# Kernel tuning notes

Measured on AMD Instinct MI355X. Metric: run time of the kernel, lower is better.

## Reference

```python
import jax, jax.numpy as jnp
import numpy as np

N = 10000      # nodes per graph
E = 160000     # random edges per graph (plus N self-loops)
IN_DIM = 4096
HID = 64       # num_hidden
H = 8          # heads
C = 5          # num_classes
SLOPE = 0.2    # LeakyReLU negative slope


def gat_conv(x, src, dst, W, al, ar, b, res_W=None):
    """DGL-style GATConv. x:(N,F) -> (N,H,D). Messages flow src->dst,
    edge softmax over in-edges of each dst node."""
    n = x.shape[0]
    h, d = al.shape
    feat = (x @ W).reshape(n, h, d)                      # (N,H,D)
    el = jnp.sum(feat * al, axis=-1)                     # (N,H)
    er = jnp.sum(feat * ar, axis=-1)                     # (N,H)
    e = jax.nn.leaky_relu(el[src] + er[dst], SLOPE)      # (E,H)
    emax = jax.ops.segment_max(e, dst, num_segments=n)   # (N,H) stable softmax
    ex = jnp.exp(e - emax[dst])
    denom = jax.ops.segment_sum(ex, dst, num_segments=n)
    alpha = ex / denom[dst]                              # (E,H)
    out = jax.ops.segment_sum(feat[src] * alpha[..., None], dst, num_segments=n)
    if res_W is not None:
        out = out + (x @ res_W).reshape(n, h, d)         # residual projection
    return out + b.reshape(h, d)


def encoder(x, src, dst, W0, al0, ar0, b0, W1, al1, ar1, b1):
    h0 = jax.nn.elu(gat_conv(x, src, dst, W0, al0, ar0, b0))   # (N,H,D)
    h0 = h0.reshape(h0.shape[0], -1)                           # flatten(1)
    return jax.nn.elu(gat_conv(h0, src, dst, W1, al1, ar1, b1))


def setup_inputs() -> dict:
    key = jax.random.key(0)
    ks = list(jax.random.split(key, 40))
    ki = iter(ks)

    def edges(k):
        k1, k2 = jax.random.split(k)
        loop = jnp.arange(N, dtype=jnp.int32)
        s = jnp.concatenate([jax.random.randint(k1, (E,), 0, N, dtype=jnp.int32), loop])
        d = jnp.concatenate([jax.random.randint(k2, (E,), 0, N, dtype=jnp.int32), loop])
        return s, d

    inp = {}
    for name in ("s0", "s1", "t"):
        s, d = edges(next(ki))
        inp[f"src_{name}"], inp[f"dst_{name}"] = s, d
    inp["features_s0"] = jax.random.normal(next(ki), (N, IN_DIM), jnp.float32)
    inp["features_s1"] = jax.random.normal(next(ki), (N, IN_DIM), jnp.float32)
    inp["features_t"]  = jax.random.normal(next(ki), (N, IN_DIM), jnp.float32)

    def lin(k, fan_in, fan_out):
        return jax.random.normal(k, (fan_in, fan_out), jnp.float32) / np.sqrt(fan_in)

    inp["W0"] = lin(next(ki), IN_DIM, H * HID)
    inp["al0"] = 0.1 * jax.random.normal(next(ki), (H, HID), jnp.float32)
    inp["ar0"] = 0.1 * jax.random.normal(next(ki), (H, HID), jnp.float32)
    inp["b0"] = jnp.zeros((H * HID,), jnp.float32)
    inp["W1"] = lin(next(ki), H * HID, H * HID)
    inp["al1"] = 0.1 * jax.random.normal(next(ki), (H, HID), jnp.float32)
    inp["ar1"] = 0.1 * jax.random.normal(next(ki), (H, HID), jnp.float32)
    inp["b1"] = jnp.zeros((H * HID,), jnp.float32)
    for k_idx in (0, 1):
        inp[f"Wc{k_idx}"] = lin(next(ki), H * HID, H * C)
        inp[f"alc{k_idx}"] = 0.1 * jax.random.normal(next(ki), (H, C), jnp.float32)
        inp[f"arc{k_idx}"] = 0.1 * jax.random.normal(next(ki), (H, C), jnp.float32)
        inp[f"bc{k_idx}"] = jnp.zeros((H * C,), jnp.float32)
        inp[f"rW{k_idx}"] = lin(next(ki), H * HID, H * C)
    inp["num_source"] = 2
    return inp


def reference(features_s0, features_s1, features_t,
              W0, al0, ar0, b0, W1, al1, ar1, b1,
              Wc0, alc0, arc0, bc0, rW0,
              Wc1, alc1, arc1, bc1, rW1,
              src_s0, dst_s0, src_s1, dst_s1, src_t, dst_t,
              num_source):
    enc_p = (W0, al0, ar0, b0, W1, al1, ar1, b1)
    cls_p = [(Wc0, alc0, arc0, bc0, rW0), (Wc1, alc1, arc1, bc1, rW1)]
    feats = [features_s0, features_s1]
    graphs = [(src_s0, dst_s0), (src_s1, dst_s1)]

    # shared-weight encoder on each source graph
    h_s = [encoder(feats[i], graphs[i][0], graphs[i][1], *enc_p)
           for i in range(num_source)]                    # each (N,H,HID)
    # per-source classifiers on their own graphs, mean over heads
    pred_s = []
    for i in range(num_source):
        Wc, alc, arc, bc, rW = cls_p[i]
        s, d = graphs[i]
        logits = gat_conv(h_s[i].reshape(N, -1), s, d, Wc, alc, arc, bc, res_W=rW)
        pred_s.append(logits.mean(axis=1))               # (N,C)
    emb_s = [h.reshape(N, -1) for h in h_s]

    # target: every source classifier applied to the target graph
    h_t = encoder(features_t, src_t, dst_t, *enc_p)
    pred_t = []
    for i in range(num_source):
        Wc, alc, arc, bc, rW = cls_p[i]
        logits = gat_conv(h_t.reshape(N, -1), src_t, dst_t, Wc, alc, arc, bc, res_W=rW)
        pred_t.append(logits.mean(axis=1))
    emb_t = h_t.reshape(N, -1)

    return (pred_s[0], pred_s[1], pred_t[0], pred_t[1], emb_s[0], emb_s[1], emb_t)
```

## Files before the change

### kernel.cpp

```cpp
#include <hip/hip_runtime.h>
#include <stdint.h>

typedef _Float16 f16;
typedef _Float16 f16x2 __attribute__((ext_vector_type(2)));
typedef _Float16 f16x8 __attribute__((ext_vector_type(8)));
typedef float f32x4 __attribute__((ext_vector_type(4)));

#define AS1 __attribute__((address_space(1)))
#define AS3 __attribute__((address_space(3)))

#define NN 10000
#define NP 10112
#define KK0 4096
#define FF 512

__global__ void k_count_b(const int* __restrict__ d0, const int* __restrict__ d1,
                          const int* __restrict__ d2, int E0, int E1, int E2,
                          int nb0, int nb1, int* __restrict__ deg){
  int b = blockIdx.x;
  const int* d; int Eg, base, lb;
  if (b < nb0){ d=d0; Eg=E0; base=0; lb=b; }
  else if (b < nb0+nb1){ d=d1; Eg=E1; base=NN; lb=b-nb0; }
  else { d=d2; Eg=E2; base=2*NN; lb=b-nb0-nb1; }
  int i = lb*256 + threadIdx.x;
  if (i < Eg) atomicAdd(&deg[base + d[i]], 1);
}

__global__ __launch_bounds__(1024) void k_scan_b(const int* __restrict__ deg_all,
    int* __restrict__ rowptr_all, int* __restrict__ cursor_all){
  int g = blockIdx.x;
  const int* deg = deg_all + g*NN;
  int* rowptr = rowptr_all + g*(NN+1);
  int* cursor = cursor_all + g*NN;
  __shared__ int ps[1024];
  int t = threadIdx.x;
  const int CH = 16;
  int i0 = t*CH;
  int sum = 0;
  for (int k=0;k<CH;k++){ int i=i0+k; if (i<NN) sum += deg[i]; }
  ps[t]=sum; __syncthreads();
  for (int off=1; off<1024; off<<=1){
    int v = (t>=off)? ps[t-off] : 0;
    __syncthreads();
    ps[t] += v;
    __syncthreads();
  }
  int run = ps[t]-sum;
  for (int k=0;k<CH;k++){
    int i=i0+k;
    if (i<=NN) rowptr[i]=run;
    if (i<NN){ cursor[i]=run; run += deg[i]; }
  }
}

__global__ void k_fill_b(const int* __restrict__ s0, const int* __restrict__ d0,
                         const int* __restrict__ s1, const int* __restrict__ d1,
                         const int* __restrict__ s2, const int* __restrict__ d2,
                         int E0, int E1, int E2, int nb0, int nb1,
                         int* __restrict__ cursor_all,
                         int* __restrict__ c0, int* __restrict__ c1, int* __restrict__ c2){
  int b = blockIdx.x;
  const int *s, *d; int Eg, lb; int* cur; int* col;
  if (b < nb0){ s=s0; d=d0; Eg=E0; lb=b; cur=cursor_all; col=c0; }
  else if (b < nb0+nb1){ s=s1; d=d1; Eg=E1; lb=b-nb0; cur=cursor_all+NN; col=c1; }
  else { s=s2; d=d2; Eg=E2; lb=b-nb0-nb1; cur=cursor_all+2*NN; col=c2; }
  int i = lb*256 + threadIdx.x;
  if (i >= Eg) return;
  int slot = atomicAdd(&cur[d[i]], 1);
  col[slot] = s[i];
}

__global__ void k_transpose_t(const float* __restrict__ W, f16* __restrict__ WT,
                              int K, int Nc){
  __shared__ float tile[32][33];
  int n0 = blockIdx.x*32, k0 = blockIdx.y*32;
  int tx = threadIdx.x, ty = threadIdx.y;
  #pragma unroll
  for (int i=0;i<32;i+=8)
    tile[ty+i][tx] = W[(long)(k0+ty+i)*Nc + n0+tx];
  __syncthreads();
  #pragma unroll
  for (int i=0;i<32;i+=8)
    WT[(long)(n0+ty+i)*K + k0+tx] = (f16)tile[tx][ty+i];
}

__global__ void k_pack_wc(const float* __restrict__ Wc, const float* __restrict__ rW,
                          f16* __restrict__ WT){
  int idx = blockIdx.x*256 + threadIdx.x;
  if (idx >= 128*512) return;
  int n = idx >> 9; int k = idx & 511;
  float v = 0.f;
  if (n < 40) v = Wc[k*40 + n];
  else if (n < 80) v = rW[k*40 + (n-40)];
  WT[idx] = (f16)v;
}

template<bool CVT>
__global__ __launch_bounds__(512,1) void k_gemmw(
    const void* __restrict__ A0v, const void* __restrict__ A1v, const void* __restrict__ A2v,
    f16* __restrict__ C0, f16* __restrict__ C1, f16* __restrict__ C2,
    const f16* __restrict__ B,
    const float* __restrict__ alp, const float* __restrict__ arp,
    float* __restrict__ elp, float* __restrict__ erp)
{
  constexpr int K = CVT ? KK0 : FF;
  constexpr int nt = K >> 6;
  __shared__ f16 lds[2][40960];

  const int nwg = gridDim.x;
  const int qd = nwg>>3, rd = nwg&7;
  const int xcd = blockIdx.x & 7, bx = blockIdx.x >> 3;
  const int wid = (xcd < rd ? xcd*(qd+1) : rd*(qd+1) + (xcd-rd)*qd) + bx;
  const int task = wid / 79;
  const int tr = wid - task*79;

  f16* C = task==0?C0:(task==1?C1:C2);

  const int t = threadIdx.x;
  const int wave = t >> 6, lane = t & 63;
  const int slot = (lane&7) ^ (lane>>3);
  const int arow0 = t >> 3;
  const int ak8 = t & 7;

  #define GLDSB_H(kt, buf, half) { \
    int ko = (kt)*64; \
    _Pragma("unroll") \
    for (int i=(half)*4; i<(half)*4+4; i++){ \
      int br = i*64 + wave*8 + (lane>>3); \
      __builtin_amdgcn_global_load_lds((const AS1 void*)(B + (long)br*K + ko + slot*8), \
          (AS3 void*)(&lds[buf][8192 + i*4096 + wave*512]), 16, 0, 0); \
    } }
  #define GLDSB(kt, buf) { GLDSB_H(kt, buf, 0); GLDSB_H(kt, buf, 1); }

  int abyte[2][8], bbyte[2][4];
  #pragma unroll
  for (int ks=0;ks<2;ks++){
    #pragma unroll
    for (int m=0;m<8;m++){
      int row = m*16 + (lane&15);
      abyte[ks][m] = row*128 + (((ks*4 + (lane>>4))*16) ^ ((row&7)<<4));
    }
    #pragma unroll
    for (int n=0;n<4;n++){
      int brow = wave*64 + n*16 + (lane&15);
      bbyte[ks][n] = 16384 + brow*128 + (((ks*4 + (lane>>4))*16) ^ ((brow&7)<<4));
    }
  }

  f32x4 zero4 = {0.f,0.f,0.f,0.f};
  f32x4 acc[8][4];
  #pragma unroll
  for (int m=0;m<8;m++)
    #pragma unroll
    for (int n=0;n<4;n++) acc[m][n] = zero4;

  #define MFMA_KS(buf, ks) { \
    const char* Ls = (const char*)&lds[buf][0]; \
    f16x8 bf[4]; \
    _Pragma("unroll") \
    for (int n=0;n<4;n++) bf[n] = *(const f16x8*)(Ls + bbyte[ks][n]); \
    _Pragma("unroll") \
    for (int m=0;m<8;m++){ \
      f16x8 af = *(const f16x8*)(Ls + abyte[ks][m]); \
      _Pragma("unroll") \
      for (int n=0;n<4;n++) \
        acc[m][n] = __builtin_amdgcn_mfma_f32_16x16x32_f16(af, bf[n], acc[m][n], 0, 0, 0); \
    } }

  int cur = 0;
  if constexpr (CVT){
    const float* Af = task==0?(const float*)A0v:(task==1?(const float*)A1v:(const float*)A2v);
    const float* gA[2];
    bool okA[2];
    #pragma unroll
    for (int s=0;s<2;s++){
      int grow = tr*128 + arow0 + s*64;
      okA[s] = grow < NN;
      gA[s] = Af + (long)(okA[s] ? grow : 0)*KK0 + ak8*8;
    }
    f32x4 arE[2][2];

    #define LOADA(kt) { \
      _Pragma("unroll") \
      for (int s=0;s<2;s++){ \
        arE[s][0] = *(const f32x4*)(gA[s] + (kt)*64); \
        arE[s][1] = *(const f32x4*)(gA[s] + (kt)*64 + 4); \
      } }
    #define WRITEA(buf) { \
      _Pragma("unroll") \
      for (int s=0;s<2;s++){ \
        int row = arow0 + s*64; \
        f16x8 v; \
        _Pragma("unroll") \
        for (int j=0;j<4;j++){ \
          v[j]   = okA[s] ? (f16)arE[s][0][j] : (f16)0.f; \
          v[4+j] = okA[s] ? (f16)arE[s][1][j] : (f16)0.f; \
        } \
        *(f16x8*)(&lds[buf][row*64 + ((ak8 ^ (arow0&7))*8)]) = v; \
      } }

    LOADA(0);
    __builtin_amdgcn_sched_barrier(0);
    GLDSB(0, 0);
    __builtin_amdgcn_sched_barrier(0);
    WRITEA(0);
    __builtin_amdgcn_sched_barrier(0);
    LOADA(1);
    __builtin_amdgcn_sched_barrier(0);
    asm volatile("s_waitcnt vmcnt(4) lgkmcnt(0)" ::: "memory");
    __builtin_amdgcn_s_barrier();
    __builtin_amdgcn_sched_barrier(0);

    for (int kt=0; kt<nt; kt++){
      if (kt+1 < nt){
        GLDSB_H(kt+1, cur^1, 0);
        __builtin_amdgcn_sched_barrier(0);
        WRITEA(cur^1);
        __builtin_amdgcn_sched_barrier(0);
      }
      __builtin_amdgcn_s_setprio(1);
      MFMA_KS(cur, 0);
      __builtin_amdgcn_s_setprio(0);
      __builtin_amdgcn_sched_barrier(0);
      if (kt+1 < nt){
        GLDSB_H(kt+1, cur^1, 1);
        __builtin_amdgcn_sched_barrier(0);
      }
      if (kt+2 < nt){
        LOADA(kt+2);
        __builtin_amdgcn_sched_barrier(0);
      }
      __builtin_amdgcn_s_setprio(1);
      MFMA_KS(cur, 1);
      __builtin_amdgcn_s_setprio(0);
      __builtin_amdgcn_sched_barrier(0);
      if (kt+1 < nt){
        if (kt+2 < nt)
          asm volatile("s_waitcnt vmcnt(4) lgkmcnt(0)" ::: "memory");
        else
          asm volatile("s_waitcnt vmcnt(0) lgkmcnt(0)" ::: "memory");
        __builtin_amdgcn_s_barrier();
        __builtin_amdgcn_sched_barrier(0);
      }
      cur ^= 1;
    }
    #undef LOADA
    #undef WRITEA
  } else {
    const f16* Ah = task==0?(const f16*)A0v:(task==1?(const f16*)A1v:(const f16*)A2v);
    const f16* Ab = Ah + (long)tr*128*K;
    const int r8 = lane>>3;

    #define GLDSA(kt, buf) { \
      _Pragma("unroll") \
      for (int s=0;s<2;s++){ \
        int arow = wave*8 + r8 + s*64; \
        __builtin_amdgcn_global_load_lds((const AS1 void*)(Ab + (long)arow*K + (kt)*64 + slot*8), \
            (AS3 void*)(&lds[buf][s*4096 + wave*512]), 16, 0, 0); \
      } }

    GLDSA(0, 0);
    GLDSB(0, 0);
    __syncthreads();
    for (int kt=0; kt<nt; kt++){
      if (kt+1 < nt){
        GLDSA(kt+1, cur^1);
        GLDSB(kt+1, cur^1);
      }
      MFMA_KS(cur, 0);
      MFMA_KS(cur, 1);
      __syncthreads();
      cur ^= 1;
    }
    #undef GLDSA
  }
  #undef GLDSB
  #undef GLDSB_H
  #undef MFMA_KS

  #pragma unroll
  for (int m=0;m<8;m++){
    int row0 = tr*128 + m*16 + ((lane>>4)<<2);
    #pragma unroll
    for (int n=0;n<4;n++){
      int col = wave*64 + n*16 + (lane&15);
      #pragma unroll
      for (int q2=0;q2<4;q2++)
        C[(long)(row0+q2)*FF + col] = (f16)acc[m][n][q2];
    }
  }

  {
    const int head = wave;
    const float* alh = alp + head*64;
    const float* arh = arp + head*64;
    float alv[4], arv[4];
    #pragma unroll
    for (int n=0;n<4;n++){ int d = n*16 + (lane&15); alv[n]=alh[d]; arv[n]=arh[d]; }
    float* elo = elp + (long)task*NN*8;
    float* ero = erp + (long)task*NN*8;
    #pragma unroll
    for (int m=0;m<8;m++){
      float e0,e1,e2,e3,r0,r1,r2,r3;
      #pragma unroll
      for (int qq=0;qq<4;qq++){
        float e=0.f, rr=0.f;
        #pragma unroll
        for (int n=0;n<4;n++){ e += acc[m][n][qq]*alv[n]; rr += acc[m][n][qq]*arv[n]; }
        #pragma unroll
        for (int off=1; off<16; off<<=1){ e += __shfl_xor(e, off); rr += __shfl_xor(rr, off); }
        if (qq==0){e0=e;r0=rr;} else if (qq==1){e1=e;r1=rr;} else if (qq==2){e2=e;r2=rr;} else {e3=e;r3=rr;}
      }
      int qq = lane&15;
      if (qq < 4){
        int node = tr*128 + m*16 + ((lane>>4)<<2) + qq;
        if (node < NN){
          float ev = qq==0?e0:(qq==1?e1:(qq==2?e2:e3));
          float rv = qq==0?r0:(qq==1?r1:(qq==2?r2:r3));
          long o = (long)node*8 + head;
          elo[o] = ev;
          ero[o] = rv;
        }
      }
    }
  }
}

struct GemmTasks { const f16* A[4]; const f16* B[4]; f16* C[4]; };

__global__ __launch_bounds__(256,3) void k_gemmb(GemmTasks p, int ntpb, int ntn,
                                                 int Nc, int K){
  __shared__ f16 lds[2][12288];
  const int bid = blockIdx.x;
  const int task = bid / ntpb;
  const int orig = bid - task*ntpb;
  const int q = ntpb >> 3, r = ntpb & 7;
  const int xcd = orig & 7, bx = orig >> 3;
  const int wid = (xcd < r ? xcd*(q+1) : r*(q+1) + (xcd-r)*q) + bx;
  const int tr = wid / ntn, tc = wid - tr*ntn;

  const f16* A = p.A[task];
  const f16* B = p.B[task];
  f16* C = p.C[task];

  const int t = threadIdx.x;
  const int wave = t >> 6, lane = t & 63;
  const int wr = wave >> 1, wc = wave & 1;

  const f16* Ab = A + (long)tr*64*K;
  const f16* Bb = B + (long)tc*128*K;

  const int slot = (lane&7) ^ (lane>>3);
  const int rbase = wave*8 + (lane>>3);

  f32x4 zero4 = {0.f,0.f,0.f,0.f};
  f32x4 acc[2][4];
  #pragma unroll
  for (int m=0;m<2;m++)
    #pragma unroll
    for (int n=0;n<4;n++) acc[m][n] = zero4;

  int abyte[2][2], bbyte[2][4];
  #pragma unroll
  for (int ks=0;ks<2;ks++){
    #pragma unroll
    for (int m=0;m<2;m++){
      int row = wr*32 + m*16 + (lane&15);
      abyte[ks][m] = row*128 + (((ks*4 + (lane>>4))*16) ^ ((row&7)<<4));
    }
    #pragma unroll
    for (int n=0;n<4;n++){
      int brow = wc*64 + n*16 + (lane&15);
      bbyte[ks][n] = 8192 + brow*128 + (((ks*4 + (lane>>4))*16) ^ ((brow&7)<<4));
    }
  }

  const int nt = K >> 6;
  int cur = 0;

  #pragma unroll
  for (int i=0;i<2;i++)
    __builtin_amdgcn_global_load_lds((const AS1 void*)(Ab + (i*32+rbase)*K + slot*8),
        (AS3 void*)(&lds[0][i*2048 + wave*512]), 16, 0, 0);
  #pragma unroll
  for (int i=0;i<4;i++)
    __builtin_amdgcn_global_load_lds((const AS1 void*)(Bb + (i*32+rbase)*K + slot*8),
        (AS3 void*)(&lds[0][4096 + i*2048 + wave*512]), 16, 0, 0);
  __syncthreads();

  for (int kt=0; kt<nt; kt++){
    if (kt+1 < nt){
      int ko = (kt+1)<<6;
      #pragma unroll
      for (int i=0;i<2;i++)
        __builtin_amdgcn_global_load_lds((const AS1 void*)(Ab + ko + (i*32+rbase)*K + slot*8),
            (AS3 void*)(&lds[cur^1][i*2048 + wave*512]), 16, 0, 0);
      #pragma unroll
      for (int i=0;i<4;i++)
        __builtin_amdgcn_global_load_lds((const AS1 void*)(Bb + ko + (i*32+rbase)*K + slot*8),
            (AS3 void*)(&lds[cur^1][4096 + i*2048 + wave*512]), 16, 0, 0);
    }
    const char* Ls = (const char*)&lds[cur][0];
    #pragma unroll
    for (int ks=0;ks<2;ks++){
      f16x8 af[2], bf[4];
      #pragma unroll
      for (int m=0;m<2;m++) af[m] = *(const f16x8*)(Ls + abyte[ks][m]);
      #pragma unroll
      for (int n=0;n<4;n++) bf[n] = *(const f16x8*)(Ls + bbyte[ks][n]);
      #pragma unroll
      for (int m=0;m<2;m++)
        #pragma unroll
        for (int n=0;n<4;n++)
          acc[m][n] = __builtin_amdgcn_mfma_f32_16x16x32_f16(af[m], bf[n], acc[m][n], 0, 0, 0);
    }
    __syncthreads();
    cur ^= 1;
  }

  #pragma unroll
  for (int m=0;m<2;m++){
    int row0 = tr*64 + wr*32 + m*16 + ((lane>>4)<<2);
    #pragma unroll
    for (int n=0;n<4;n++){
      int col = tc*128 + wc*64 + n*16 + (lane&15);
      #pragma unroll
      for (int q2=0;q2<4;q2++)
        C[(long)(row0+q2)*Nc + col] = (f16)acc[m][n][q2];
    }
  }
}

#define MAXD 128

struct AggArgs {
  const int* rp[3]; const int* cs[3];
  const float* el; const float* er;
  const f16* feat[3];
  const float* bias;
  f16* outH[3];
  float* outF[3];
};

__global__ __launch_bounds__(256) void k_agg_b(AggArgs a){
  int b = blockIdx.x;
  int g = b / NN, n = b - g*NN;
  const int* rowptr = a.rp[g];
  const int* colsrc = a.cs[g];
  const float* el = a.el + (long)g*NN*8;
  const f16* featH = a.feat[g];
  int t = threadIdx.x;
  __shared__ float sm[MAXD*8];
  __shared__ int   scol[MAXD];
  __shared__ float red[256];
  __shared__ float inv[8];
  __shared__ float ern[8];
  if (t < 8) ern[t] = a.er[((long)g*NN+n)*8+t];
  __syncthreads();
  int j0 = rowptr[n], deg = rowptr[n+1]-j0;
  int h2 = t >> 5;
  int c = t*2;
  float a0=0.f, a1=0.f;

  if (deg <= MAXD){
    {
      int h = t & 7;
      float dsum = 0.f;
      for (int jj = t>>3; jj < deg; jj += 32){
        int s = colsrc[j0+jj];
        float v = el[s*8+h] + ern[h];
        v = (v>0.f)? v : 0.2f*v;
        float ex = __expf(v);
        dsum += ex;
        sm[jj*8+h] = ex;
        if (h==0) scol[jj] = s;
      }
      red[t] = dsum; __syncthreads();
      if (t<128) red[t] += red[t+128]; __syncthreads();
      if (t<64)  red[t] += red[t+64];  __syncthreads();
      if (t<32)  red[t] += red[t+32];  __syncthreads();
      if (t<16)  red[t] += red[t+16];  __syncthreads();
      if (t<8)   inv[t] = 1.0f / (red[t] + red[t+8]);
      __syncthreads();
    }
    float ivh = inv[h2];
    int jj = 0;
    for (; jj+4<=deg; jj+=4){
      int s0=scol[jj], s1=scol[jj+1], s2=scol[jj+2], s3=scol[jj+3];
      float x0=sm[(jj+0)*8+h2], x1=sm[(jj+1)*8+h2], x2=sm[(jj+2)*8+h2], x3=sm[(jj+3)*8+h2];
      f16x2 f0 = *(const f16x2*)(featH + (long)s0*FF + c);
      f16x2 f1 = *(const f16x2*)(featH + (long)s1*FF + c);
      f16x2 f2 = *(const f16x2*)(featH + (long)s2*FF + c);
      f16x2 f3 = *(const f16x2*)(featH + (long)s3*FF + c);
      a0 += x0*(float)f0[0] + x1*(float)f1[0] + x2*(float)f2[0] + x3*(float)f3[0];
      a1 += x0*(float)f0[1] + x1*(float)f1[1] + x2*(float)f2[1] + x3*(float)f3[1];
    }
    for (; jj<deg; jj++){
      int s = scol[jj];
      float x = sm[jj*8+h2];
      f16x2 f = *(const f16x2*)(featH + (long)s*FF + c);
      a0 += x*(float)f[0];
      a1 += x*(float)f[1];
    }
    a0 *= ivh; a1 *= ivh;
  } else {
    {
      int h = t & 7;
      float dsum = 0.f;
      for (int jj = t>>3; jj < deg; jj += 32){
        int s = colsrc[j0+jj];
        float v = el[s*8+h] + ern[h];
        v = (v>0.f)? v : 0.2f*v;
        float ex = __expf(v);
        dsum += ex;
        if (jj < MAXD){
          sm[jj*8+h] = ex;
          if (h==0) scol[jj] = s;
        }
      }
      red[t] = dsum; __syncthreads();
      if (t<128) red[t] += red[t+128]; __syncthreads();
      if (t<64)  red[t] += red[t+64];  __syncthreads();
      if (t<32)  red[t] += red[t+32];  __syncthreads();
      if (t<16)  red[t] += red[t+16];  __syncthreads();
      if (t<8)   inv[t] = 1.0f / (red[t] + red[t+8]);
      __syncthreads();
    }
    float ivh = inv[h2];
    for (int jj=0; jj<deg; jj++){
      int s; float ex;
      if (jj < MAXD){ s = scol[jj]; ex = sm[jj*8+h2]; }
      else {
        s = colsrc[j0+jj];
        float v = el[s*8+h2] + ern[h2];
        v = (v>0.f)? v : 0.2f*v;
        ex = __expf(v);
      }
      float alpha = ex * ivh;
      f16x2 f = *(const f16x2*)(featH + (long)s*FF + c);
      a0 += alpha*(float)f[0];
      a1 += alpha*(float)f[1];
    }
  }

  a0 += a.bias[c]; a1 += a.bias[c+1];
  a0 = (a0>0.f)? a0 : __expf(a0)-1.f;
  a1 = (a1>0.f)? a1 : __expf(a1)-1.f;
  f16x2 o; o[0]=(f16)a0; o[1]=(f16)a1;
  *(f16x2*)(a.outH[g] + (long)n*FF + c) = o;
  float* oF = a.outF[g];
  if (oF){
    oF[(long)n*FF + c]     = a0;
    oF[(long)n*FF + c + 1] = a1;
  }
}

__global__ void k_elerc_b(const f16* __restrict__ fc,
    const float* __restrict__ alc0, const float* __restrict__ arc0,
    const float* __restrict__ alc1, const float* __restrict__ arc1,
    float* __restrict__ el, float* __restrict__ er){
  int idx = blockIdx.x*256 + threadIdx.x;
  if (idx >= 4*NN*8) return;
  int ti = idx / (NN*8);
  int rem = idx - ti*NN*8;
  int n = rem>>3, hh = rem&7;
  const f16* featc = fc + (long)ti*NP*128;
  const float* al = (ti&1) ? alc1 : alc0;
  const float* ar_ = (ti&1) ? arc1 : arc0;
  float a=0.f, bsum=0.f;
  #pragma unroll
  for (int cc=0; cc<5; cc++){
    float v = (float)featc[(long)n*128 + hh*5 + cc];
    a += v*al[hh*5+cc];
    bsum += v*ar_[hh*5+cc];
  }
  el[idx]=a; er[idx]=bsum;
}

struct ClsArgs {
  const int* rp[3]; const int* cs[3];
  const float* el; const float* er;
  const f16* fc;
  const float* bc[2];
  float* pred;
};

__global__ __launch_bounds__(64) void k_cls_b(ClsArgs a){
  int b = blockIdx.x;
  int ti = b / NN, n = b - ti*NN;
  int g = ti<2 ? ti : 2;
  int ci = ti&1;
  const int* rowptr = a.rp[g];
  const int* colsrc = a.cs[g];
  const float* el = a.el + (long)ti*NN*8;
  const f16* featc = a.fc + (long)ti*NP*128;
  const float* bc = a.bc[ci];
  float* pred = a.pred + (long)ti*5*NN;
  int l = threadIdx.x;
  __shared__ float sm[MAXD*8];
  __shared__ int   scol[MAXD];
  __shared__ float inv[8];
  __shared__ float ern[8];
  __shared__ float lg[40];
  if (l<8) ern[l] = a.er[((long)ti*NN+n)*8+l];
  __syncthreads();
  int j0 = rowptr[n], deg = rowptr[n+1]-j0;

  if (deg <= MAXD){
    {
      int h = l & 7;
      float dsum = 0.f;
      for (int jj = l>>3; jj < deg; jj += 8){
        int s = colsrc[j0+jj];
        float v = el[s*8+h] + ern[h];
        v = (v>0.f)? v : 0.2f*v;
        float ex = __expf(v);
        dsum += ex;
        sm[jj*8+h] = ex;
        if (h==0) scol[jj] = s;
      }
      dsum += __shfl_xor(dsum, 8);
      dsum += __shfl_xor(dsum, 16);
      dsum += __shfl_xor(dsum, 32);
      if (l<8) inv[l] = 1.0f/dsum;
    }
    __syncthreads();
    if (l<40){
      int h = l/5;
      float ivh = inv[h];
      float acc = 0.f;
      int jj = 0;
      for (; jj+4<=deg; jj+=4){
        int s0=scol[jj], s1=scol[jj+1], s2=scol[jj+2], s3=scol[jj+3];
        float x0=sm[(jj+0)*8+h], x1=sm[(jj+1)*8+h], x2=sm[(jj+2)*8+h], x3=sm[(jj+3)*8+h];
        float v0=(float)featc[(long)s0*128 + l];
        float v1=(float)featc[(long)s1*128 + l];
        float v2=(float)featc[(long)s2*128 + l];
        float v3=(float)featc[(long)s3*128 + l];
        acc += x0*v0 + x1*v1 + x2*v2 + x3*v3;
      }
      for (; jj<deg; jj++)
        acc += sm[jj*8+h] * (float)featc[(long)scol[jj]*128 + l];
      acc *= ivh;
      acc += (float)featc[(long)n*128 + 40 + l];
      acc += bc[l];
      lg[l] = acc;
    }
  } else {
    {
      int h = l & 7;
      float dsum = 0.f;
      for (int jj = l>>3; jj < deg; jj += 8){
        int s = colsrc[j0+jj];
        float v = el[s*8+h] + ern[h];
        v = (v>0.f)? v : 0.2f*v;
        float ex = __expf(v);
        dsum += ex;
        if (jj < MAXD){
          sm[jj*8+h] = ex;
          if (h==0) scol[jj] = s;
        }
      }
      dsum += __shfl_xor(dsum, 8);
      dsum += __shfl_xor(dsum, 16);
      dsum += __shfl_xor(dsum, 32);
      if (l<8) inv[l] = 1.0f/dsum;
    }
    __syncthreads();
    if (l<40){
      int h = l/5;
      float ivh = inv[h];
      float acc = 0.f;
      for (int jj=0; jj<deg; jj++){
        int s; float ex;
        if (jj < MAXD){ s = scol[jj]; ex = sm[jj*8+h]; }
        else {
          s = colsrc[j0+jj];
          float v = el[s*8+h] + ern[h];
          v = (v>0.f)? v : 0.2f*v;
          ex = __expf(v);
        }
        acc += ex*ivh * (float)featc[(long)s*128 + l];
      }
      acc += (float)featc[(long)n*128 + 40 + l];
      acc += bc[l];
      lg[l] = acc;
    }
  }
  __syncthreads();
  if (l<5){
    float p=0.f;
    #pragma unroll
    for (int h=0;h<8;h++) p += lg[h*5+l];
    pred[(long)n*5 + l] = p*0.125f;
  }
}

extern "C" void kernel_launch(void* const* d_in, const int* in_sizes, int n_in,
                              void* d_out, int out_size, void* d_ws, size_t ws_size,
                              hipStream_t stream){
  const int* srcs[3] = {(const int*)d_in[0], (const int*)d_in[2], (const int*)d_in[4]};
  const int* dsts[3] = {(const int*)d_in[1], (const int*)d_in[3], (const int*)d_in[5]};
  int E[3] = {in_sizes[0], in_sizes[2], in_sizes[4]};
  const float* X[3] = {(const float*)d_in[6], (const float*)d_in[7], (const float*)d_in[8]};
  const float* W0  = (const float*)d_in[9];
  const float* al0 = (const float*)d_in[10];
  const float* ar0 = (const float*)d_in[11];
  const float* b0  = (const float*)d_in[12];
  const float* W1  = (const float*)d_in[13];
  const float* al1 = (const float*)d_in[14];
  const float* ar1 = (const float*)d_in[15];
  const float* b1  = (const float*)d_in[16];
  const float* Wcv[2] = {(const float*)d_in[17], (const float*)d_in[22]};
  const float* alc[2] = {(const float*)d_in[18], (const float*)d_in[23]};
  const float* arc[2] = {(const float*)d_in[19], (const float*)d_in[24]};
  const float* bcv[2] = {(const float*)d_in[20], (const float*)d_in[25]};
  const float* rWv[2] = {(const float*)d_in[21], (const float*)d_in[26]};

  float* out = (float*)d_out;
  float* embOut[3] = {out+200000, out+200000+(long)NN*FF, out+200000+2L*NN*FF};

  char* w = (char*)d_ws;
  size_t off = 0;
  auto alloc = [&](size_t bytes)->void*{
    void* p = (void*)(w + off);
    off += (bytes + 255) & ~((size_t)255);
    return p;
  };
  f16* W0T = (f16*)alloc((size_t)FF*KK0*2);
  f16* W1T = (f16*)alloc((size_t)FF*FF*2);
  f16* WcT[2] = {(f16*)alloc(128*512*2), (f16*)alloc(128*512*2)};
  f16* feat0H[3], *h0H[3], *feat1H[3], *embH[3];
  for (int g=0;g<3;g++) feat0H[g] = (f16*)alloc((size_t)NP*FF*2);
  for (int g=0;g<3;g++) h0H[g]    = (f16*)alloc((size_t)NP*FF*2);
  for (int g=0;g<3;g++) feat1H[g] = (f16*)alloc((size_t)NP*FF*2);
  for (int g=0;g<3;g++) embH[g]   = (f16*)alloc((size_t)NP*FF*2);
  f16* featc = (f16*)alloc((size_t)4*NP*128*2);
  float* el_e = (float*)alloc((size_t)3*NN*8*4);
  float* er_e = (float*)alloc((size_t)3*NN*8*4);
  float* el_c = (float*)alloc((size_t)4*NN*8*4);
  float* er_c = (float*)alloc((size_t)4*NN*8*4);
  int* deg    = (int*)alloc((size_t)3*NN*4);
  int* cursor = (int*)alloc((size_t)3*NN*4);
  int* rowptr = (int*)alloc((size_t)3*(NN+1)*4);
  int* colsrc[3];
  for (int g=0;g<3;g++) colsrc[g] = (int*)alloc((size_t)E[g]*4);
  (void)ws_size; (void)n_in; (void)out_size;

  int nb[3] = {(E[0]+255)/256, (E[1]+255)/256, (E[2]+255)/256};
  hipMemsetAsync(deg, 0, (size_t)3*NN*4, stream);
  k_count_b<<<nb[0]+nb[1]+nb[2], 256, 0, stream>>>(dsts[0], dsts[1], dsts[2],
      E[0], E[1], E[2], nb[0], nb[1], deg);
  k_scan_b<<<3, 1024, 0, stream>>>(deg, rowptr, cursor);
  k_fill_b<<<nb[0]+nb[1]+nb[2], 256, 0, stream>>>(srcs[0], dsts[0], srcs[1], dsts[1],
      srcs[2], dsts[2], E[0], E[1], E[2], nb[0], nb[1], cursor,
      colsrc[0], colsrc[1], colsrc[2]);

  k_transpose_t<<<dim3(FF/32, KK0/32), dim3(32,8), 0, stream>>>(W0, W0T, KK0, FF);
  k_transpose_t<<<dim3(FF/32, FF/32), dim3(32,8), 0, stream>>>(W1, W1T, FF, FF);
  k_pack_wc<<<(128*512+255)/256, 256, 0, stream>>>(Wcv[0], rWv[0], WcT[0]);
  k_pack_wc<<<(128*512+255)/256, 256, 0, stream>>>(Wcv[1], rWv[1], WcT[1]);

  const int* rp[3] = {rowptr, rowptr+(NN+1), rowptr+2*(NN+1)};

  k_gemmw<true><<<237, 512, 0, stream>>>(X[0], X[1], X[2],
      feat0H[0], feat0H[1], feat0H[2], W0T, al0, ar0, el_e, er_e);
  {
    AggArgs a;
    for (int g=0;g<3;g++){ a.rp[g]=rp[g]; a.cs[g]=colsrc[g]; a.feat[g]=feat0H[g];
                           a.outH[g]=h0H[g]; a.outF[g]=nullptr; }
    a.el = el_e; a.er = er_e; a.bias = b0;
    k_agg_b<<<3*NN, 256, 0, stream>>>(a);
  }

  k_gemmw<false><<<237, 512, 0, stream>>>(h0H[0], h0H[1], h0H[2],
      feat1H[0], feat1H[1], feat1H[2], W1T, al1, ar1, el_e, er_e);
  {
    AggArgs a;
    for (int g=0;g<3;g++){ a.rp[g]=rp[g]; a.cs[g]=colsrc[g]; a.feat[g]=feat1H[g];
                           a.outH[g]=embH[g]; a.outF[g]=embOut[g]; }
    a.el = el_e; a.er = er_e; a.bias = b1;
    k_agg_b<<<3*NN, 256, 0, stream>>>(a);
  }

  {
    GemmTasks p;
    const int tg[4] = {0,1,2,2};
    for (int i=0;i<4;i++){ p.A[i]=embH[tg[i]]; p.B[i]=WcT[i&1]; p.C[i]=featc + (long)i*NP*128; }
    k_gemmb<<<4*158, 256, 0, stream>>>(p, 158, 1, 128, FF);
  }
  k_elerc_b<<<(4*NN*8+255)/256, 256, 0, stream>>>(featc, alc[0], arc[0], alc[1], arc[1], el_c, er_c);
  {
    ClsArgs a;
    for (int g=0;g<3;g++){ a.rp[g]=rp[g]; a.cs[g]=colsrc[g]; }
    a.el = el_c; a.er = er_c; a.fc = featc;
    a.bc[0] = bcv[0]; a.bc[1] = bcv[1];
    a.pred = out;
    k_cls_b<<<4*NN, 64, 0, stream>>>(a);
  }
}
```

Measured before the change: 512.2 us.

## Load GEMM B operand directly into registers instead of staging through LDS

The weight (B) tiles are now read from global memory straight into MFMA operand registers, double-buffered across two register sets, rather than copied into LDS via global_load_lds. This shrinks shared memory per block from about 160KB to 32KB and removes LDS reads for B. The aim is to cut LDS traffic and footprint. The cost is more VGPRs, uncoalesced 16-byte global reads of B per lane, and the loss of the explicit sched_barrier/setprio interleaving. The waitcnt logic is also simplified, and it is not obvious that the global loads into bfr are waited on correctly before use.

```diff
diff --git a/kernel.cpp b/kernel.cpp
--- a/kernel.cpp
+++ b/kernel.cpp
@@ -105,7 +105,7 @@
 {
   constexpr int K = CVT ? KK0 : FF;
   constexpr int nt = K >> 6;
-  __shared__ f16 lds[2][40960];
+  __shared__ f16 lds[2][8192];
 
   const int nwg = gridDim.x;
   const int qd = nwg>>3, rd = nwg&7;
@@ -122,29 +122,26 @@
   const int arow0 = t >> 3;
   const int ak8 = t & 7;
 
-  #define GLDSB_H(kt, buf, half) { \
-    int ko = (kt)*64; \
+  int boff[2][4];
+  #pragma unroll
+  for (int ks=0;ks<2;ks++)
+    #pragma unroll
+    for (int n=0;n<4;n++)
+      boff[ks][n] = ((wave*64 + n*16 + (lane&15))*K + ks*32 + ((lane>>4)*8))*2;
+
+  #define BLOAD(kt, SET) { \
     _Pragma("unroll") \
-    for (int i=(half)*4; i<(half)*4+4; i++){ \
-      int br = i*64 + wave*8 + (lane>>3); \
-      __builtin_amdgcn_global_load_lds((const AS1 void*)(B + (long)br*K + ko + slot*8), \
-          (AS3 void*)(&lds[buf][8192 + i*4096 + wave*512]), 16, 0, 0); \
-    } }
-  #define GLDSB(kt, buf) { GLDSB_H(kt, buf, 0); GLDSB_H(kt, buf, 1); }
-
-  int abyte[2][8], bbyte[2][4];
-  #pragma unroll
-  for (int ks=0;ks<2;ks++){
-    #pragma unroll
-    for (int m=0;m<8;m++){
-      int row = m*16 + (lane&15);
-      abyte[ks][m] = row*128 + (((ks*4 + (lane>>4))*16) ^ ((row&7)<<4));
-    }
-    #pragma unroll
-    for (int n=0;n<4;n++){
-      int brow = wave*64 + n*16 + (lane&15);
-      bbyte[ks][n] = 16384 + brow*128 + (((ks*4 + (lane>>4))*16) ^ ((brow&7)<<4));
-    }
+    for (int ks=0;ks<2;ks++) \
+      _Pragma("unroll") \
+      for (int n=0;n<4;n++) \
+        SET[ks][n] = *(const f16x8*)((const char*)B + boff[ks][n] + (kt)*128); \
+    }
+
+  int abyte[8];
+  #pragma unroll
+  for (int m=0;m<8;m++){
+    int row = m*16 + (lane&15);
+    abyte[m] = row*128 + (((lane>>4)*16) ^ ((row&7)<<4));
   }
 
   f32x4 zero4 = {0.f,0.f,0.f,0.f};
@@ -154,17 +151,19 @@
     #pragma unroll
     for (int n=0;n<4;n++) acc[m][n] = zero4;
 
-  #define MFMA_KS(buf, ks) { \
+  f16x8 bfr0[2][4], bfr1[2][4];
+
+  #define MFMA_T(buf, SET) { \
     const char* Ls = (const char*)&lds[buf][0]; \
-    f16x8 bf[4]; \
     _Pragma("unroll") \
-    for (int n=0;n<4;n++) bf[n] = *(const f16x8*)(Ls + bbyte[ks][n]); \
-    _Pragma("unroll") \
-    for (int m=0;m<8;m++){ \
-      f16x8 af = *(const f16x8*)(Ls + abyte[ks][m]); \
+    for (int ks=0;ks<2;ks++){ \
       _Pragma("unroll") \
-      for (int n=0;n<4;n++) \
-        acc[m][n] = __builtin_amdgcn_mfma_f32_16x16x32_f16(af, bf[n], acc[m][n], 0, 0, 0); \
+      for (int m=0;m<8;m++){ \
+        f16x8 af = *(const f16x8*)(Ls + (abyte[m] ^ (ks*64))); \
+        _Pragma("unroll") \
+        for (int n=0;n<4;n++) \
+          acc[m][n] = __builtin_amdgcn_mfma_f32_16x16x32_f16(af, SET[ks][n], acc[m][n], 0, 0, 0); \
+      } \
     } }
 
   int cur = 0;
@@ -200,50 +199,27 @@
       } }
 
     LOADA(0);
-    __builtin_amdgcn_sched_barrier(0);
-    GLDSB(0, 0);
-    __builtin_amdgcn_sched_barrier(0);
+    BLOAD(0, bfr0);
     WRITEA(0);
-    __builtin_amdgcn_sched_barrier(0);
     LOADA(1);
-    __builtin_amdgcn_sched_barrier(0);
-    asm volatile("s_waitcnt vmcnt(4) lgkmcnt(0)" ::: "memory");
+    asm volatile("s_waitcnt lgkmcnt(0)" ::: "memory");
     __builtin_amdgcn_s_barrier();
-    __builtin_amdgcn_sched_barrier(0);
-
-    for (int kt=0; kt<nt; kt++){
-      if (kt+1 < nt){
-        GLDSB_H(kt+1, cur^1, 0);
-        __builtin_amdgcn_sched_barrier(0);
-        WRITEA(cur^1);
-        __builtin_amdgcn_sched_barrier(0);
-      }
-      __builtin_amdgcn_s_setprio(1);
-      MFMA_KS(cur, 0);
-      __builtin_amdgcn_s_setprio(0);
-      __builtin_amdgcn_sched_barrier(0);
-      if (kt+1 < nt){
-        GLDSB_H(kt+1, cur^1, 1);
-        __builtin_amdgcn_sched_barrier(0);
-      }
-      if (kt+2 < nt){
-        LOADA(kt+2);
-        __builtin_amdgcn_sched_barrier(0);
-      }
-      __builtin_amdgcn_s_setprio(1);
-      MFMA_KS(cur, 1);
-      __builtin_amdgcn_s_setprio(0);
-      __builtin_amdgcn_sched_barrier(0);
-      if (kt+1 < nt){
-        if (kt+2 < nt)
-          asm volatile("s_waitcnt vmcnt(4) lgkmcnt(0)" ::: "memory");
-        else
-          asm volatile("s_waitcnt vmcnt(0) lgkmcnt(0)" ::: "memory");
-        __builtin_amdgcn_s_barrier();
-        __builtin_amdgcn_sched_barrier(0);
-      }
-      cur ^= 1;
-    }
+
+    #define ITER_CVT(kt, SETCUR, SETNXT) { \
+      if ((kt)+1 < nt){ BLOAD((kt)+1, SETNXT); WRITEA(cur^1); } \
+      if ((kt)+2 < nt){ LOADA((kt)+2); } \
+      MFMA_T(cur, SETCUR); \
+      if ((kt)+1 < nt){ \
+        asm volatile("s_waitcnt lgkmcnt(0)" ::: "memory"); \
+        __builtin_amdgcn_s_barrier(); \
+      } \
+      cur ^= 1; }
+
+    for (int kt=0; kt<nt; kt+=2){
+      ITER_CVT(kt,   bfr0, bfr1);
+      ITER_CVT(kt+1, bfr1, bfr0);
+    }
+    #undef ITER_CVT
     #undef LOADA
     #undef WRITEA
   } else {
@@ -260,23 +236,28 @@
       } }
 
     GLDSA(0, 0);
-    GLDSB(0, 0);
-    __syncthreads();
-    for (int kt=0; kt<nt; kt++){
-      if (kt+1 < nt){
-        GLDSA(kt+1, cur^1);
-        GLDSB(kt+1, cur^1);
-      }
-      MFMA_KS(cur, 0);
-      MFMA_KS(cur, 1);
-      __syncthreads();
-      cur ^= 1;
-    }
+    BLOAD(0, bfr0);
+    asm volatile("s_waitcnt vmcnt(8) lgkmcnt(0)" ::: "memory");
+    __builtin_amdgcn_s_barrier();
+
+    #define ITER_H(kt, SETCUR, SETNXT) { \
+      if ((kt)+1 < nt){ GLDSA((kt)+1, cur^1); BLOAD((kt)+1, SETNXT); } \
+      MFMA_T(cur, SETCUR); \
+      if ((kt)+1 < nt){ \
+        asm volatile("s_waitcnt vmcnt(8) lgkmcnt(0)" ::: "memory"); \
+        __builtin_amdgcn_s_barrier(); \
+      } \
+      cur ^= 1; }
+
+    for (int kt=0; kt<nt; kt+=2){
+      ITER_H(kt,   bfr0, bfr1);
+      ITER_H(kt+1, bfr1, bfr0);
+    }
+    #undef ITER_H
     #undef GLDSA
   }
-  #undef GLDSB
-  #undef GLDSB_H
-  #undef MFMA_KS
+  #undef BLOAD
+  #undef MFMA_T
 
   #pragma unroll
   for (int m=0;m<8;m++){
```

Measured after the change: 768.9 us. 1.5x slower.
